# Performance work log

Hardware: AMD Instinct MI355X
Metric: run time of the kernel (lower is better)

Reference implementation:

```python
import jax, jax.numpy as jnp
import numpy as np

B, S, D, H = 4, 2048, 1024, 16
HD = D // H  # 64


def setup_inputs() -> dict:
    key = jax.random.key(0)
    k1, k2, k3, k4, k5 = jax.random.split(key, 5)
    scale = 0.02
    return {
        "hidden_states": jax.random.normal(k1, (B, S, D), dtype=jnp.float32),
        "c_attn_w": jax.random.normal(k2, (D, 3 * D), dtype=jnp.float32) * scale,
        "c_attn_b": jax.random.normal(k3, (3 * D,), dtype=jnp.float32) * scale,
        "c_proj_w": jax.random.normal(k4, (D, D), dtype=jnp.float32) * scale,
        "c_proj_b": jax.random.normal(k5, (D,), dtype=jnp.float32) * scale,
    }


def reference(hidden_states, c_attn_w, c_attn_b, c_proj_w, c_proj_b):
    b, s, d = hidden_states.shape
    # Conv1D: x @ W + b, fused QKV
    qkv = hidden_states @ c_attn_w + c_attn_b  # [b, s, 3d]
    q, k, v = jnp.split(qkv, 3, axis=-1)
    # split heads -> [b, h, s, hd]
    def split_heads(x):
        return x.reshape(b, s, H, HD).transpose(0, 2, 1, 3)
    q, k, v = split_heads(q), split_heads(k), split_heads(v)
    # scaled dot-product attention with causal mask (eager GPT-2 math)
    scores = jnp.einsum("bhqd,bhkd->bhqk", q, k) / jnp.asarray(HD ** 0.5, q.dtype)
    causal = jnp.tril(jnp.ones((s, s), dtype=bool))  # [s, s]
    mask_value = jnp.asarray(jnp.finfo(scores.dtype).min, scores.dtype)
    scores = jnp.where(causal[None, None, :, :], scores, mask_value)
    attn = jax.nn.softmax(scores, axis=-1)
    out = jnp.einsum("bhqk,bhkd->bhqd", attn, v)  # [b, h, s, hd]
    out = out.transpose(0, 2, 1, 3).reshape(b, s, d)  # merge heads
    out = out @ c_proj_w + c_proj_b
    return out
```

## Files before the change

### kernel.cpp

```cpp
#include <hip/hip_runtime.h>
#include <hip/hip_bf16.h>
#include <stdint.h>

#define B_ 4
#define S_ 2048
#define D_ 1024
#define H_ 16
#define HD_ 64

typedef __bf16 bf16_t;
typedef bf16_t bf16x8 __attribute__((ext_vector_type(8)));
typedef bf16_t bf16x4 __attribute__((ext_vector_type(4)));
typedef float f32x4 __attribute__((ext_vector_type(4)));
typedef float f32x16 __attribute__((ext_vector_type(16)));

__device__ __forceinline__ bf16x8 cvt8(f32x4 lo, f32x4 hi) {
  bf16x8 r;
#pragma unroll
  for (int i = 0; i < 4; i++) {
    r[i] = (bf16_t)lo[i];
    r[i + 4] = (bf16_t)hi[i];
  }
  return r;
}

__device__ __forceinline__ void async_lds16(const bf16_t* g, bf16_t* l) {
  __builtin_amdgcn_global_load_lds(
      (const __attribute__((address_space(1))) void*)g,
      (__attribute__((address_space(3))) void*)l, 16, 0, 0);
}

__device__ __forceinline__ uint32_t pk2(float a, float b) {
  union {
    bf16_t h[2];
    uint32_t u;
  } x;
  x.h[0] = (bf16_t)a;
  x.h[1] = (bf16_t)b;
  return x.u;
}

__device__ __forceinline__ void swap32(uint32_t& a, uint32_t& b) {
  asm("v_permlane32_swap_b32 %0, %1" : "+v"(a), "+v"(b));
}

union PAU {
  uint32_t w[4];
  bf16x8 v;
};

__global__ __launch_bounds__(256) void prep(
    const float* __restrict__ hidden, bf16_t* __restrict__ hb,
    const float* __restrict__ attn_w, bf16_t* __restrict__ wT1) {
  __shared__ bf16_t tile[32][33];
  const int bid = blockIdx.x;
  if (bid < 4096) {
    size_t i = ((size_t)bid * 256 + threadIdx.x) * 8;
    f32x4 lo = *(const f32x4*)(hidden + i);
    f32x4 hi = *(const f32x4*)(hidden + i + 4);
    *(bf16x8*)(hb + i) = cvt8(lo, hi);
  } else {
    const int b2 = bid - 4096;
    const int c0 = (b2 % 96) * 32, r0 = (b2 / 96) * 32;
    const int tx = threadIdx.x & 31, ty = threadIdx.x >> 5;
    const int R = 1024, C = 3072;
    for (int i = ty; i < 32; i += 8)
      tile[i][tx] = (bf16_t)attn_w[(size_t)(r0 + i) * C + c0 + tx];
    __syncthreads();
    for (int i = ty; i < 32; i += 8)
      wT1[(size_t)(c0 + i) * R + r0 + tx] = tile[tx][i];
  }
}

__global__ void transpose_cvt(const float* __restrict__ in,
                              bf16_t* __restrict__ out, int R, int C) {
  __shared__ bf16_t tile[32][33];
  int c0 = blockIdx.x * 32, r0 = blockIdx.y * 32;
  int tx = threadIdx.x, ty = threadIdx.y;
  for (int i = ty; i < 32; i += 8)
    tile[i][tx] = (bf16_t)in[(size_t)(r0 + i) * C + c0 + tx];
  __syncthreads();
  for (int i = ty; i < 32; i += 8)
    out[(size_t)(c0 + i) * R + r0 + tx] = tile[tx][i];
}

__global__ __launch_bounds__(256) void gemm_bt(
    const void* __restrict__ A, const bf16_t* __restrict__ BT,
    const float* __restrict__ bias, float* __restrict__ Cout,
    bf16_t* __restrict__ qws, bf16_t* __restrict__ kws,
    bf16_t* __restrict__ vws, int M, int Nw, int K, int mode, int a_is_f32,
    size_t a_off) {
  __shared__ bf16_t As[128 * 32];
  __shared__ bf16_t Bs[128 * 32];
  const int tid = threadIdx.x;
  const int wave = tid >> 6, lane = tid & 63;
  const int quad = lane >> 4, tn = lane & 15;
  const int lid = blockIdx.y * gridDim.x + blockIdx.x;
  const int cpx = (gridDim.x * gridDim.y) >> 3;
  const int nl = (lid & 7) * cpx + (lid >> 3);
  const int m_blk = (nl / gridDim.x) * 128, n_blk = (nl % gridDim.x) * 128;
  const int wm = (wave >> 1) * 64, wn = (wave & 1) * 64;

  f32x4 acc[4][4] = {};

  const int srow = wave * 32 + (lane >> 2);
  const int scol = (lane & 3) * 8;
  size_t aoff = a_off + (size_t)(m_blk + srow) * K + scol;
  const bf16_t* gb = BT + (size_t)(n_blk + srow) * K + scol;
  bf16_t* lbB0 = &Bs[wave * 1024];
  bf16_t* lbB1 = &Bs[wave * 1024 + 512];
  bf16_t* laA0 = &As[wave * 1024];
  bf16_t* laA1 = &As[wave * 1024 + 512];

  for (int k0 = 0; k0 < K; k0 += 32) {
    async_lds16(gb, lbB0);
    async_lds16(gb + (size_t)16 * K, lbB1);
    if (a_is_f32) {
      const float* gaf = (const float*)A + aoff;
      f32x4 a00 = *(const f32x4*)gaf;
      f32x4 a01 = *(const f32x4*)(gaf + 4);
      f32x4 a10 = *(const f32x4*)(gaf + (size_t)16 * K);
      f32x4 a11 = *(const f32x4*)(gaf + (size_t)16 * K + 4);
      *(bf16x8*)&As[srow * 32 + scol] = cvt8(a00, a01);
      *(bf16x8*)&As[(srow + 16) * 32 + scol] = cvt8(a10, a11);
    } else {
      const bf16_t* ga = (const bf16_t*)A + aoff;
      async_lds16(ga, laA0);
      async_lds16(ga + (size_t)16 * K, laA1);
    }
    aoff += 32;
    gb += 32;
    __syncthreads();

    bf16x8 af[4], bfr[4];
#pragma unroll
    for (int i = 0; i < 4; i++)
      af[i] = *(const bf16x8*)&As[(wm + i * 16 + tn) * 32 + quad * 8];
#pragma unroll
    for (int i = 0; i < 4; i++)
      bfr[i] = *(const bf16x8*)&Bs[(wn + i * 16 + tn) * 32 + quad * 8];
#pragma unroll
    for (int mi = 0; mi < 4; mi++)
#pragma unroll
      for (int ni = 0; ni < 4; ni++)
        acc[mi][ni] = __builtin_amdgcn_mfma_f32_16x16x32_bf16(af[mi], bfr[ni],
                                                              acc[mi][ni], 0, 0, 0);
    __syncthreads();
  }

  if (mode == 0) {
#pragma unroll
    for (int ni = 0; ni < 4; ni++) {
      int n = n_blk + wn + ni * 16 + tn;
      float bv = bias[n];
#pragma unroll
      for (int mi = 0; mi < 4; mi++)
#pragma unroll
        for (int r = 0; r < 4; r++) {
          int m = m_blk + wm + mi * 16 + quad * 4 + r;
          Cout[(size_t)m * Nw + n] = acc[mi][ni][r] + bv;
        }
    }
  } else {
#pragma unroll
    for (int ni = 0; ni < 4; ni++) {
      int n = n_blk + wn + ni * 16 + tn;
      int sec = n >> 10;
      int hn = n & 1023;
      int hh = hn >> 6, hd = hn & 63;
      float bv = bias[n];
      if (sec == 2) {
#pragma unroll
        for (int mi = 0; mi < 4; mi++) {
          int m = m_blk + wm + mi * 16 + quad * 4;
          int bb = m >> 11, s = m & 2047;
          bf16x4 pk;
#pragma unroll
          for (int r = 0; r < 4; r++) pk[r] = (bf16_t)(acc[mi][ni][r] + bv);
          *(bf16x4*)&vws[((size_t)(bb * H_ + hh) * HD_ + hd) * S_ + s] = pk;
        }
      } else {
        bf16_t* dst = (sec == 0) ? qws : kws;
#pragma unroll
        for (int mi = 0; mi < 4; mi++)
#pragma unroll
          for (int r = 0; r < 4; r++) {
            int m = m_blk + wm + mi * 16 + quad * 4 + r;
            int bb = m >> 11, s = m & 2047;
            dst[((size_t)(bb * H_ + hh) * S_ + s) * HD_ + hd] =
                (bf16_t)(acc[mi][ni][r] + bv);
          }
      }
    }
  }
}

__global__ __launch_bounds__(512, 2) void attn_kernel(
    const bf16_t* __restrict__ Qw, const bf16_t* __restrict__ Kw,
    const bf16_t* __restrict__ VTw, bf16_t* __restrict__ Ow) {
  __shared__ bf16_t Ks[2][128 * 64];
  __shared__ bf16_t Vt[2][64 * 128];

  const int tid = threadIdx.x;
  const int wave = tid >> 6, lane = tid & 63;
  const int lq = lane & 31;
  const int h = lane >> 5;
  const int qoff = h * 4;
  const int bid = blockIdx.x;
  const int j = bid >> 3;
  const int bh = (bid & 7) * 8 + (j >> 2);
  const int pj = j & 3;

  const bf16_t* Qb = Qw + (size_t)bh * S_ * HD_;
  const bf16_t* Kb = Kw + (size_t)bh * S_ * HD_;
  const bf16_t* VTb = VTw + (size_t)bh * HD_ * S_;

  const float kScale = 0.125f * 1.44269504088896f;

  bf16x8 onesf;
#pragma unroll
  for (int jj = 0; jj < 8; jj++) onesf[jj] = (bf16_t)1.0f;

  const float NEG = -30000.0f;
  const int b = bh >> 4, hh = bh & 15;

  const int krow = wave * 16 + (lane >> 3);
  const int ksl = lane & 7;
  const bf16_t* kpA = Kb + (size_t)krow * HD_ + ((ksl ^ (krow & 7)) * 8);
  const bf16_t* kpB =
      Kb + (size_t)(krow + 8) * HD_ + ((ksl ^ ((krow + 8) & 7)) * 8);
  const int vrow = wave * 8 + (lane >> 4);
  const int vsl = lane & 15;
  const bf16_t* vpA = VTb + (size_t)vrow * S_ + ((vsl ^ (vrow & 7)) * 8);
  const bf16_t* vpB =
      VTb + (size_t)(vrow + 4) * S_ + ((vsl ^ ((vrow + 4) & 7)) * 8);

#define STAGE(buf, kt)                                                     \
  do {                                                                     \
    async_lds16(kpA + (size_t)(kt) * (128 * HD_), &Ks[buf][wave * 1024]);  \
    async_lds16(kpB + (size_t)(kt) * (128 * HD_),                          \
                &Ks[buf][wave * 1024 + 512]);                              \
    async_lds16(vpA + (size_t)(kt) * 128, &Vt[buf][wave * 1024]);          \
    async_lds16(vpB + (size_t)(kt) * 128, &Vt[buf][wave * 1024 + 512]);    \
  } while (0)

  for (int task = 0; task < 2; task++) {
    const int qt = task == 0 ? (7 - pj) : pj;
    const int qb = qt * 256;
    const int qa = qb + ((lq >> 3) << 6) + wave * 8 + (lq & 7);

    bf16x8 qf[4];
#pragma unroll
    for (int kg = 0; kg < 4; kg++) {
      bf16x8 v = *(const bf16x8*)&Qb[(size_t)qa * HD_ + kg * 16 + h * 8];
#pragma unroll
      for (int jj = 0; jj < 8; jj++) v[jj] = (bf16_t)((float)v[jj] * kScale);
      qf[kg] = v;
    }

    f32x16 o0 = {}, o1 = {};
    f32x16 ls = {};
    float mrow = NEG;

    const int kt_max = (qb + 255) >> 7;

    if (task) __syncthreads();
    STAGE(0, 0);

    for (int kt = 0; kt <= kt_max; kt++) {
      __syncthreads();
      if (kt < kt_max) STAGE((kt + 1) & 1, kt + 1);

      const bf16_t* KsB = Ks[kt & 1];
      const bf16_t* VtB = Vt[kt & 1];
      const int rsl = lq & 7;

      f32x16 st[4] = {{}, {}, {}, {}};
      __builtin_amdgcn_s_setprio(1);
#pragma unroll
      for (int kg = 0; kg < 4; kg++) {
        const int slot = kg * 2 + h;
#pragma unroll
        for (int bk = 0; bk < 4; bk++) {
          bf16x8 kf = *(const bf16x8*)&KsB[(bk * 32 + lq) * 64 +
                                           ((slot ^ rsl) * 8)];
          st[bk] =
              __builtin_amdgcn_mfma_f32_32x32x16_bf16(kf, qf[kg], st[bk], 0, 0, 0);
        }
      }
      __builtin_amdgcn_s_setprio(0);
      if (kt * 128 + 127 > qb) {
#pragma unroll
        for (int bk = 0; bk < 4; bk++)
#pragma unroll
          for (int r = 0; r < 16; r++) {
            int key = kt * 128 + bk * 32 + (r & 3) + 8 * (r >> 2) + qoff;
            if (key > qa) st[bk][r] = NEG;
          }
      }
      float mx;
      {
        float m4[4];
#pragma unroll
        for (int bk = 0; bk < 4; bk++) {
          float a0 = fmaxf(fmaxf(st[bk][0], st[bk][1]),
                           fmaxf(st[bk][2], st[bk][3]));
          float a1 = fmaxf(fmaxf(st[bk][4], st[bk][5]),
                           fmaxf(st[bk][6], st[bk][7]));
          float a2 = fmaxf(fmaxf(st[bk][8], st[bk][9]),
                           fmaxf(st[bk][10], st[bk][11]));
          float a3 = fmaxf(fmaxf(st[bk][12], st[bk][13]),
                           fmaxf(st[bk][14], st[bk][15]));
          m4[bk] = fmaxf(fmaxf(a0, a1), fmaxf(a2, a3));
        }
        mx = fmaxf(fmaxf(m4[0], m4[1]), fmaxf(m4[2], m4[3]));
        mx = fmaxf(mx, __shfl_xor(mx, 32, 64));
      }

      if (__any(mx > mrow + 8.f)) {
        float mnew = fmaxf(mrow, mx);
        float alpha = exp2f(mrow - mnew);
        mrow = mnew;
#pragma unroll
        for (int r = 0; r < 16; r++) {
          float ar = __shfl(alpha, (r & 3) + 8 * (r >> 2) + qoff, 64);
          o0[r] *= ar;
          o1[r] *= ar;
          ls[r] *= ar;
        }
      }
#pragma unroll
      for (int bk = 0; bk < 4; bk++)
#pragma unroll
        for (int r = 0; r < 16; r++) st[bk][r] = exp2f(st[bk][r] - mrow);

      PAU pa[8];
#pragma unroll
      for (int bk = 0; bk < 4; bk++) {
        uint32_t w[8];
#pragma unroll
        for (int i = 0; i < 8; i++)
          w[i] = pk2(st[bk][2 * i], st[bk][2 * i + 1]);
        swap32(w[0], w[2]);
        swap32(w[1], w[3]);
        swap32(w[4], w[6]);
        swap32(w[5], w[7]);
        pa[2 * bk].w[0] = w[0];
        pa[2 * bk].w[1] = w[1];
        pa[2 * bk].w[2] = w[2];
        pa[2 * bk].w[3] = w[3];
        pa[2 * bk + 1].w[0] = w[4];
        pa[2 * bk + 1].w[1] = w[5];
        pa[2 * bk + 1].w[2] = w[6];
        pa[2 * bk + 1].w[3] = w[7];
      }

      __builtin_amdgcn_s_setprio(1);
#pragma unroll
      for (int kg = 0; kg < 8; kg++) {
        const int slot = kg * 2 + h;
        bf16x8 vf0 = *(const bf16x8*)&VtB[lq * 128 + ((slot ^ rsl) * 8)];
        bf16x8 vf1 =
            *(const bf16x8*)&VtB[(32 + lq) * 128 + ((slot ^ rsl) * 8)];
        o0 = __builtin_amdgcn_mfma_f32_32x32x16_bf16(pa[kg].v, vf0, o0, 0, 0, 0);
        o1 = __builtin_amdgcn_mfma_f32_32x32x16_bf16(pa[kg].v, vf1, o1, 0, 0, 0);
        ls = __builtin_amdgcn_mfma_f32_32x32x16_bf16(pa[kg].v, onesf, ls, 0, 0, 0);
      }
      __builtin_amdgcn_s_setprio(0);
    }

#pragma unroll
    for (int r = 0; r < 16; r++) {
      int qr = (r & 3) + 8 * (r >> 2) + qoff;
      int q = qb + ((qr >> 3) << 6) + wave * 8 + (qr & 7);
      float inv = 1.f / fmaxf(ls[r], 1e-30f);
      bf16_t* dst = Ow + (size_t)(b * S_ + q) * D_ + hh * HD_;
      dst[lq] = (bf16_t)(o0[r] * inv);
      dst[32 + lq] = (bf16_t)(o1[r] * inv);
    }
  }
#undef STAGE
}

extern "C" void kernel_launch(void* const* d_in, const int* in_sizes, int n_in,
                              void* d_out, int out_size, void* d_ws,
                              size_t ws_size, hipStream_t stream) {
  const float* hidden = nullptr;
  const float* attn_w = nullptr;
  const float* attn_b = nullptr;
  const float* proj_w = nullptr;
  const float* proj_b = nullptr;
  for (int i = 0; i < n_in; ++i) {
    switch (in_sizes[i]) {
      case 8388608: hidden = (const float*)d_in[i]; break;
      case 3145728: attn_w = (const float*)d_in[i]; break;
      case 3072:    attn_b = (const float*)d_in[i]; break;
      case 1048576: proj_w = (const float*)d_in[i]; break;
      case 1024:    proj_b = (const float*)d_in[i]; break;
      default: break;
    }
  }
  if (!hidden) hidden = (const float*)d_in[0];
  if (!attn_w) attn_w = (const float*)d_in[1];
  if (!attn_b) attn_b = (const float*)d_in[2];
  if (!proj_w) proj_w = (const float*)d_in[3];
  if (!proj_b) proj_b = (const float*)d_in[4];
  float* out = (float*)d_out;

  char* ws = (char*)d_ws;
  const size_t AWS_B = (size_t)B_ * S_ * D_ * 2;
  const size_t QKV_E = (size_t)B_ * H_ * S_ * HD_;

  bf16_t* aws = (bf16_t*)ws;
  bf16_t* wT1 = (bf16_t*)ws;
  bf16_t* qws = (bf16_t*)(ws + AWS_B);
  bf16_t* kws = qws + QKV_E;
  bf16_t* vws = kws + QKV_E;
  bf16_t* wT2 = qws;
  bf16_t* hb = (bf16_t*)d_out;

  prep<<<dim3(7168), 256, 0, stream>>>(hidden, hb, attn_w, wT1);
  gemm_bt<<<dim3(24, 64), 256, 0, stream>>>(
      hb, wT1, attn_b, nullptr, qws, kws, vws, 8192, 3072, 1024, 1, 0, 0);
  attn_kernel<<<dim3(256), 512, 0, stream>>>(qws, kws, vws, aws);
  transpose_cvt<<<dim3(32, 32), dim3(32, 8), 0, stream>>>(proj_w, wT2, 1024, 1024);
  gemm_bt<<<dim3(8, 64), 256, 0, stream>>>(
      aws, wT2, proj_b, out, nullptr, nullptr, nullptr, 8192, 1024, 1024, 0, 0, 0);
}
```

Measured before the change: 287.2 us.

## Double-buffer GEMM LDS tiles with K=64 steps and XOR-swizzled layout

```diff
diff --git a/kernel.cpp b/kernel.cpp
--- a/kernel.cpp
+++ b/kernel.cpp
@@ -84,14 +84,13 @@
     out[(size_t)(c0 + i) * R + r0 + tx] = tile[tx][i];
 }
 
-__global__ __launch_bounds__(256) void gemm_bt(
-    const void* __restrict__ A, const bf16_t* __restrict__ BT,
+__global__ __launch_bounds__(256, 2) void gemm_db(
+    const bf16_t* __restrict__ Ab, const bf16_t* __restrict__ BT,
     const float* __restrict__ bias, float* __restrict__ Cout,
     bf16_t* __restrict__ qws, bf16_t* __restrict__ kws,
-    bf16_t* __restrict__ vws, int M, int Nw, int K, int mode, int a_is_f32,
-    size_t a_off) {
-  __shared__ bf16_t As[128 * 32];
-  __shared__ bf16_t Bs[128 * 32];
+    bf16_t* __restrict__ vws, int M, int Nw, int K, int mode) {
+  __shared__ bf16_t As[2][128 * 64];
+  __shared__ bf16_t Bs[2][128 * 64];
   const int tid = threadIdx.x;
   const int wave = tid >> 6, lane = tid & 63;
   const int quad = lane >> 4, tn = lane & 15;
@@ -103,50 +102,65 @@
 
   f32x4 acc[4][4] = {};
 
-  const int srow = wave * 32 + (lane >> 2);
-  const int scol = (lane & 3) * 8;
-  size_t aoff = a_off + (size_t)(m_blk + srow) * K + scol;
-  const bf16_t* gb = BT + (size_t)(n_blk + srow) * K + scol;
-  bf16_t* lbB0 = &Bs[wave * 1024];
-  bf16_t* lbB1 = &Bs[wave * 1024 + 512];
-  bf16_t* laA0 = &As[wave * 1024];
-  bf16_t* laA1 = &As[wave * 1024 + 512];
-
-  for (int k0 = 0; k0 < K; k0 += 32) {
-    async_lds16(gb, lbB0);
-    async_lds16(gb + (size_t)16 * K, lbB1);
-    if (a_is_f32) {
-      const float* gaf = (const float*)A + aoff;
-      f32x4 a00 = *(const f32x4*)gaf;
-      f32x4 a01 = *(const f32x4*)(gaf + 4);
-      f32x4 a10 = *(const f32x4*)(gaf + (size_t)16 * K);
-      f32x4 a11 = *(const f32x4*)(gaf + (size_t)16 * K + 4);
-      *(bf16x8*)&As[srow * 32 + scol] = cvt8(a00, a01);
-      *(bf16x8*)&As[(srow + 16) * 32 + scol] = cvt8(a10, a11);
-    } else {
-      const bf16_t* ga = (const bf16_t*)A + aoff;
-      async_lds16(ga, laA0);
-      async_lds16(ga + (size_t)16 * K, laA1);
-    }
-    aoff += 32;
-    gb += 32;
-    __syncthreads();
-
-    bf16x8 af[4], bfr[4];
-#pragma unroll
-    for (int i = 0; i < 4; i++)
-      af[i] = *(const bf16x8*)&As[(wm + i * 16 + tn) * 32 + quad * 8];
-#pragma unroll
-    for (int i = 0; i < 4; i++)
-      bfr[i] = *(const bf16x8*)&Bs[(wn + i * 16 + tn) * 32 + quad * 8];
+  const int srowA = wave * 32 + (lane >> 3);
+  const int scolS = ((lane & 7) ^ (lane >> 3)) * 8;
+  const bf16_t* aSrc = Ab + (size_t)(m_blk + srowA) * K + scolS;
+  const bf16_t* bSrc = BT + (size_t)(n_blk + srowA) * K + scolS;
+
+#define GST(buf, jt)                                                       \
+  do {                                                                     \
+    _Pragma("unroll") for (int c = 0; c < 4; c++) {                        \
+      async_lds16(aSrc + (size_t)(jt)*64 + (size_t)c * 8 * K,              \
+                  &As[buf][(wave * 32 + c * 8) * 64]);                     \
+      async_lds16(bSrc + (size_t)(jt)*64 + (size_t)c * 8 * K,              \
+                  &Bs[buf][(wave * 32 + c * 8) * 64]);                     \
+    }                                                                      \
+  } while (0)
+
+  const int NT = K >> 6;
+  GST(0, 0);
+  GST(1, 1);
+  asm volatile("s_waitcnt vmcnt(8)" ::: "memory");
+  __builtin_amdgcn_s_barrier();
+
+  int cur = 0;
+  for (int j = 0; j < NT; ++j) {
+    bf16x8 af[4][2], bfv[4][2];
 #pragma unroll
     for (int mi = 0; mi < 4; mi++)
 #pragma unroll
-      for (int ni = 0; ni < 4; ni++)
-        acc[mi][ni] = __builtin_amdgcn_mfma_f32_16x16x32_bf16(af[mi], bfr[ni],
-                                                              acc[mi][ni], 0, 0, 0);
-    __syncthreads();
-  }
+      for (int ks = 0; ks < 2; ks++)
+        af[mi][ks] = *(const bf16x8*)&As[cur][(wm + mi * 16 + tn) * 64 +
+                                             (((ks * 4 + quad) ^ (tn & 7)) * 8)];
+#pragma unroll
+    for (int ni = 0; ni < 4; ni++)
+#pragma unroll
+      for (int ks = 0; ks < 2; ks++)
+        bfv[ni][ks] = *(const bf16x8*)&Bs[cur][(wn + ni * 16 + tn) * 64 +
+                                              (((ks * 4 + quad) ^ (tn & 7)) * 8)];
+    asm volatile("s_waitcnt lgkmcnt(0)" ::: "memory");
+    __builtin_amdgcn_s_barrier();
+    if (j + 2 < NT) GST(cur, j + 2);
+    __builtin_amdgcn_s_setprio(1);
+#pragma unroll
+    for (int ks = 0; ks < 2; ks++)
+#pragma unroll
+      for (int mi = 0; mi < 4; mi++)
+#pragma unroll
+        for (int ni = 0; ni < 4; ni++)
+          acc[mi][ni] = __builtin_amdgcn_mfma_f32_16x16x32_bf16(
+              af[mi][ks], bfv[ni][ks], acc[mi][ni], 0, 0, 0);
+    __builtin_amdgcn_s_setprio(0);
+    if (j + 1 < NT) {
+      if (j + 2 < NT)
+        asm volatile("s_waitcnt vmcnt(8)" ::: "memory");
+      else
+        asm volatile("s_waitcnt vmcnt(0)" ::: "memory");
+      __builtin_amdgcn_s_barrier();
+    }
+    cur ^= 1;
+  }
+#undef GST
 
   if (mode == 0) {
 #pragma unroll
@@ -420,10 +434,10 @@
   bf16_t* hb = (bf16_t*)d_out;
 
   prep<<<dim3(7168), 256, 0, stream>>>(hidden, hb, attn_w, wT1);
-  gemm_bt<<<dim3(24, 64), 256, 0, stream>>>(
-      hb, wT1, attn_b, nullptr, qws, kws, vws, 8192, 3072, 1024, 1, 0, 0);
+  gemm_db<<<dim3(24, 64), 256, 0, stream>>>(
+      hb, wT1, attn_b, nullptr, qws, kws, vws, 8192, 3072, 1024, 1);
   attn_kernel<<<dim3(256), 512, 0, stream>>>(qws, kws, vws, aws);
   transpose_cvt<<<dim3(32, 32), dim3(32, 8), 0, stream>>>(proj_w, wT2, 1024, 1024);
-  gemm_bt<<<dim3(8, 64), 256, 0, stream>>>(
-      aws, wT2, proj_b, out, nullptr, nullptr, nullptr, 8192, 1024, 1024, 0, 0, 0);
-}
+  gemm_db<<<dim3(8, 64), 256, 0, stream>>>(
+      aws, wT2, proj_b, out, nullptr, nullptr, nullptr, 8192, 1024, 1024, 0);
+}
```

After: 256.8 us. 1.12x faster.
